# Performance work log

Measured on AMD Instinct MI355X. Metric: run time of the kernel, lower is better.

Reference implementation:

```python
import jax, jax.numpy as jnp
import numpy as np

N_NODES = 100000  # number of bonds (nodes of the bond-graph)
N_EDGES = 500000  # angle edges per head
NUM_ANGLE = 4
BOND_DIM = 128
HIDDEN_DIM = 128  # must equal BOND_DIM (alpha * x_j elementwise)


def setup_inputs() -> dict:
    key = jax.random.key(0)
    k1, k2, k3 = jax.random.split(key, 3)
    bond_feat = jax.random.normal(k1, (N_NODES, BOND_DIM), dtype=jnp.float32)
    edge_index = jax.random.randint(k2, (NUM_ANGLE, 2, N_EDGES), 0, N_NODES, dtype=jnp.int64)
    # attn_fc weight per angle head: Linear(2*bond_dim -> hidden_dim); stored as [in, out]
    W = jax.random.normal(k3, (NUM_ANGLE, 2 * BOND_DIM, HIDDEN_DIM), dtype=jnp.float32) * (1.0 / np.sqrt(2 * BOND_DIM))
    b = jnp.zeros((NUM_ANGLE, HIDDEN_DIM), dtype=jnp.float32)
    return {"bond_feat": bond_feat, "edge_index": edge_index, "W": W, "b": b}


def reference(bond_feat, edge_index, W, b):
    n_nodes = bond_feat.shape[0]

    def one_angle(ei, Wk, bk):
        src, dst = ei[0], ei[1]            # PyG: edge_index[0]=j (source), [1]=i (target)
        x_j = bond_feat[src]               # [E, D]
        x_i = bond_feat[dst]               # [E, D]
        alpha = jnp.tanh(jnp.concatenate([x_i, x_j], axis=-1) @ Wk + bk)  # [E, H]
        msg = alpha * x_j                  # requires H == D
        return jax.ops.segment_sum(msg, dst, num_segments=n_nodes)        # [N, H]

    h = jax.vmap(one_angle)(edge_index, W, b)          # [A, N, H]
    # merge == 'cat': concat heads along feature dim -> [N, A*H]
    feat_h = jnp.transpose(h, (1, 0, 2)).reshape(n_nodes, -1)
    return feat_h
```

## Files before the change

kernel.cpp:

```cpp
#include <hip/hip_runtime.h>
#include <hip/hip_bf16.h>
#include <stdint.h>

#define NN 100000
#define NE 500000
#define NA 4
#define DIM 128
#define LDA 136

#define NBINS (NA * NN)
#define SCAN_CHUNK 1024
#define NBLK ((NBINS + SCAN_CHUNK - 1) / SCAN_CHUNK)

typedef __attribute__((ext_vector_type(8))) short bf16x8;
typedef __attribute__((ext_vector_type(4))) float f32x4;
typedef unsigned short u16;
typedef unsigned int u32;
typedef unsigned long long u64;

__device__ __forceinline__ u16 f2bf(float x) {
    u32 u = __float_as_uint(x);
    u32 r = (u + 0x7fffu + ((u >> 16) & 1u)) >> 16;
    return (u16)r;
}
__device__ __forceinline__ float bf2f(u16 h) {
    return __uint_as_float(((u32)h) << 16);
}
__device__ __forceinline__ float fast_tanh(float x) {
    float t = __expf(2.0f * x);
    return 1.0f - __fdividef(2.0f, t + 1.0f);
}

__global__ __launch_bounds__(256) void cast_bond(const float* __restrict__ x,
                                                 u16* __restrict__ y) {
    int i = blockIdx.x * 256 + threadIdx.x;
    if (i >= NN * DIM / 8) return;
    const float4* xv = (const float4*)x;
    float4 a = xv[2 * i], b = xv[2 * i + 1];
    uint4 o;
    o.x = (u32)f2bf(a.x) | ((u32)f2bf(a.y) << 16);
    o.y = (u32)f2bf(a.z) | ((u32)f2bf(a.w) << 16);
    o.z = (u32)f2bf(b.x) | ((u32)f2bf(b.y) << 16);
    o.w = (u32)f2bf(b.z) | ((u32)f2bf(b.w) << 16);
    ((uint4*)y)[i] = o;
}

__global__ __launch_bounds__(256) void pack_w(const float* __restrict__ W,
                                              u16* __restrict__ WbT) {
    int i = blockIdx.x * 256 + threadIdx.x;
    int d = i & 127;
    int o = (i >> 7) & 127;
    int st = i >> 14;
    WbT[i] = f2bf(W[(size_t)(st * 128 + d) * 128 + o]);
}

__global__ __launch_bounds__(256) void gemm_y(const u16* __restrict__ bondB,
                                              const u16* __restrict__ WbT,
                                              const float* __restrict__ bias,
                                              u16* __restrict__ Y) {
    __shared__ __align__(16) u16 As[64 * LDA];
    __shared__ __align__(16) u16 Bs[128 * LDA];
    const int node0 = blockIdx.x * 64;
    const int tid = threadIdx.x;

#pragma unroll
    for (int it = 0; it < 4; ++it) {
        int idx = it * 256 + tid;
        int row = idx >> 4, ch = idx & 15;
        int gr = node0 + row;
        if (gr >= NN) gr = NN - 1;
        *(uint4*)&As[row * LDA + ch * 8] = *(const uint4*)&bondB[(size_t)gr * DIM + ch * 8];
    }

    const int wave = tid >> 6, lane = tid & 63;
    const int m0 = wave * 16;
    const int lrow = lane & 15;
    const int lk8 = (lane >> 4) * 8;
    const int rbase = (lane >> 4) * 4;

    for (int slab = 0; slab < 8; ++slab) {
        __syncthreads();
        const u16* Wslab = WbT + (size_t)slab * DIM * DIM;
#pragma unroll
        for (int it = 0; it < 8; ++it) {
            int idx = it * 256 + tid;
            *(uint4*)&Bs[(idx >> 4) * LDA + (idx & 15) * 8] = *(const uint4*)&Wslab[idx * 8];
        }
        __syncthreads();

        f32x4 acc[8] = {};
#pragma unroll
        for (int kk = 0; kk < 4; ++kk) {
            int ko = kk * 32 + lk8;
            bf16x8 a = *(const bf16x8*)&As[(m0 + lrow) * LDA + ko];
#pragma unroll
            for (int nb = 0; nb < 8; ++nb) {
                bf16x8 b = *(const bf16x8*)&Bs[(nb * 16 + lrow) * LDA + ko];
                acc[nb] = __builtin_amdgcn_mfma_f32_16x16x32_bf16(a, b, acc[nb], 0, 0, 0);
            }
        }

        const int k = slab >> 1, t = slab & 1;
#pragma unroll
        for (int nb = 0; nb < 8; ++nb) {
            int o = nb * 16 + lrow;
            float bv = (t == 0) ? bias[k * DIM + o] : 0.0f;
#pragma unroll
            for (int r = 0; r < 4; ++r) {
                int node = node0 + m0 + rbase + r;
                if (node < NN)
                    Y[(size_t)slab * NN * DIM + (size_t)node * DIM + o] = f2bf(acc[nb][r] + bv);
            }
        }
    }
}


__global__ __launch_bounds__(256) void hist_kernel(const int* __restrict__ ei,
                                                   int* __restrict__ counts) {
    int k = blockIdx.y;
    int e = blockIdx.x * 256 + threadIdx.x;
    if (e >= NE) return;
    int dst = ei[(size_t)(k * 2 + 1) * NE + e];
    atomicAdd(&counts[k * NN + dst], 1);
}

__global__ __launch_bounds__(256) void scan_reduce(const int* __restrict__ counts,
                                                   int* __restrict__ blockSums) {
    int b = blockIdx.x, t = threadIdx.x;
    int base = b * SCAN_CHUNK + t * 4;
    int s = 0;
#pragma unroll
    for (int u = 0; u < 4; ++u) {
        int i = base + u;
        if (i < NBINS) s += counts[i];
    }
    __shared__ int red[256];
    red[t] = s;
    __syncthreads();
    for (int off = 128; off > 0; off >>= 1) {
        if (t < off) red[t] += red[t + off];
        __syncthreads();
    }
    if (t == 0) blockSums[b] = red[0];
}

__global__ void scan_bases(int* __restrict__ blockSums, int* __restrict__ offsets) {
    __shared__ int lds[512];
    int t = threadIdx.x;
    lds[t] = (t < NBLK) ? blockSums[t] : 0;
    __syncthreads();
    if (t == 0) {
        int run = 0;
        for (int i = 0; i < NBLK; ++i) {
            int v = lds[i];
            lds[i] = run;
            run += v;
        }
        offsets[NBINS] = run;
    }
    __syncthreads();
    if (t < NBLK) blockSums[t] = lds[t];
}

__global__ __launch_bounds__(256) void scan_write(const int* __restrict__ counts,
                                                  const int* __restrict__ blockBases,
                                                  int* __restrict__ offsets,
                                                  int* __restrict__ woff) {
    int b = blockIdx.x, t = threadIdx.x;
    int base = b * SCAN_CHUNK + t * 4;
    int v[4];
    int s = 0;
#pragma unroll
    for (int u = 0; u < 4; ++u) {
        int i = base + u;
        v[u] = (i < NBINS) ? counts[i] : 0;
        s += v[u];
    }
    __shared__ int lds[256];
    lds[t] = s;
    __syncthreads();
    for (int off = 1; off < 256; off <<= 1) {
        int add = (t >= off) ? lds[t - off] : 0;
        __syncthreads();
        lds[t] += add;
        __syncthreads();
    }
    int run = blockBases[b] + lds[t] - s;
#pragma unroll
    for (int u = 0; u < 4; ++u) {
        int i = base + u;
        if (i < NBINS) {
            offsets[i] = run;
            woff[i] = run;
            run += v[u];
        }
    }
}

__global__ __launch_bounds__(256) void scatter_kernel(const int* __restrict__ ei,
                                                      int* __restrict__ woff,
                                                      int* __restrict__ sorted_src) {
    int k = blockIdx.y;
    int e = blockIdx.x * 256 + threadIdx.x;
    if (e >= NE) return;
    int src = ei[(size_t)(k * 2 + 0) * NE + e];
    int dst = ei[(size_t)(k * 2 + 1) * NE + e];
    int pos = atomicAdd(&woff[k * NN + dst], 1);
    sorted_src[pos] = src;
}

__global__ __launch_bounds__(256) void gather_kernel(const int* __restrict__ offsets,
                                                     const int* __restrict__ sorted_src,
                                                     const u16* __restrict__ Y,
                                                     const u16* __restrict__ bondB,
                                                     float* __restrict__ out) {
    const int k = blockIdx.y;
    const int node = blockIdx.x * 4 + (threadIdx.x >> 6);
    const int lane = threadIdx.x & 63;
    const int f = lane * 2;
    const int bin = k * NN + node;

    int base = __builtin_amdgcn_readfirstlane(offsets[bin]);
    int cnt = __builtin_amdgcn_readfirstlane(offsets[bin + 1]) - base;

    const u16* __restrict__ Y1p = Y + (size_t)(2 * k) * NN * DIM;
    const u16* __restrict__ Y2p = Y + (size_t)(2 * k + 1) * NN * DIM;

    const u32 y1 = *(const u32*)&Y1p[(u32)node * DIM + f];
    const float y1a = __uint_as_float(y1 << 16);
    const float y1b = __uint_as_float(y1 & 0xffff0000u);
    float acc0 = 0.0f, acc1 = 0.0f;

#define EDGE(w, x)                                                      \
    {                                                                   \
        float p0 = y1a + __uint_as_float((w) << 16);                    \
        float p1 = y1b + __uint_as_float((w) & 0xffff0000u);            \
        float e0 = __expf(2.0f * p0);                                   \
        float e1 = __expf(2.0f * p1);                                   \
        float d0 = e0 + 1.0f;                                           \
        float d1 = e1 + 1.0f;                                           \
        float r = __fdividef(1.0f, d0 * d1);                            \
        float th0 = fmaf(-2.0f * d1, r, 1.0f);                          \
        float th1 = fmaf(-2.0f * d0, r, 1.0f);                          \
        acc0 = fmaf(th0, __uint_as_float((x) << 16), acc0);             \
        acc1 = fmaf(th1, __uint_as_float((x) & 0xffff0000u), acc1);     \
    }

    while (cnt > 0) {
        const int take = (cnt < 64) ? cnt : 64;
        const int srcl = sorted_src[base + ((lane < take) ? lane : (take - 1))];
        int e = 0;
        for (; e + 4 <= take; e += 4) {
            const int s0 = __builtin_amdgcn_readlane(srcl, e);
            const int s1 = __builtin_amdgcn_readlane(srcl, e + 1);
            const int s2 = __builtin_amdgcn_readlane(srcl, e + 2);
            const int s3 = __builtin_amdgcn_readlane(srcl, e + 3);
            const u32 w0 = *(const u32*)&Y2p[(u32)s0 * DIM + f];
            const u32 x0 = *(const u32*)&bondB[(u32)s0 * DIM + f];
            const u32 w1 = *(const u32*)&Y2p[(u32)s1 * DIM + f];
            const u32 x1 = *(const u32*)&bondB[(u32)s1 * DIM + f];
            const u32 w2 = *(const u32*)&Y2p[(u32)s2 * DIM + f];
            const u32 x2 = *(const u32*)&bondB[(u32)s2 * DIM + f];
            const u32 w3 = *(const u32*)&Y2p[(u32)s3 * DIM + f];
            const u32 x3 = *(const u32*)&bondB[(u32)s3 * DIM + f];
            EDGE(w0, x0);
            EDGE(w1, x1);
            EDGE(w2, x2);
            EDGE(w3, x3);
        }
        for (; e < take; ++e) {
            const int s = __builtin_amdgcn_readlane(srcl, e);
            const u32 w = *(const u32*)&Y2p[(u32)s * DIM + f];
            const u32 x = *(const u32*)&bondB[(u32)s * DIM + f];
            EDGE(w, x);
        }
        base += take;
        cnt -= take;
    }
#undef EDGE

    u64 uv = ((u64)__float_as_uint(acc1) << 32) | (u64)__float_as_uint(acc0);
    __builtin_nontemporal_store(uv, (u64*)(out + (size_t)node * (NA * DIM) + k * DIM + f));
}

__global__ __launch_bounds__(256) void edge_kernel(const int* __restrict__ ei,
                                                   const u16* __restrict__ Y,
                                                   const float* __restrict__ bond,
                                                   float* __restrict__ out) {
    const int k = blockIdx.y;
    const int e = blockIdx.x * 4 + (threadIdx.x >> 6);
    const int lane = threadIdx.x & 63;
    const int src = ei[(size_t)(k * 2 + 0) * NE + e];
    const int dst = ei[(size_t)(k * 2 + 1) * NE + e];
    const int f = lane * 2;
    const u32 y1p = *(const u32*)&Y[((size_t)(k * 2 + 0) * NN + dst) * DIM + f];
    const u32 y2p = *(const u32*)&Y[((size_t)(k * 2 + 1) * NN + src) * DIM + f];
    const float2 xj = *(const float2*)&bond[(size_t)src * DIM + f];
    float p0 = bf2f((u16)(y1p & 0xffffu)) + bf2f((u16)(y2p & 0xffffu));
    float p1 = bf2f((u16)(y1p >> 16)) + bf2f((u16)(y2p >> 16));
    float a0 = fast_tanh(p0);
    float a1 = fast_tanh(p1);
    float* op = out + (size_t)dst * (NA * DIM) + k * DIM + f;
    atomicAdd(op, a0 * xj.x);
    atomicAdd(op + 1, a1 * xj.y);
}

__global__ __launch_bounds__(128) void fallback_edge(const float* __restrict__ bond,
                                                     const int* __restrict__ ei,
                                                     const float* __restrict__ W,
                                                     const float* __restrict__ bias,
                                                     float* __restrict__ out) {
    __shared__ float xi[DIM], xj[DIM];
    const int k = blockIdx.y;
    const int e = blockIdx.x;
    const int o = threadIdx.x;
    const int src = ei[(size_t)(k * 2 + 0) * NE + e];
    const int dst = ei[(size_t)(k * 2 + 1) * NE + e];
    xi[o] = bond[(size_t)dst * DIM + o];
    xj[o] = bond[(size_t)src * DIM + o];
    __syncthreads();
    const float* Wk = W + (size_t)k * 2 * DIM * DIM;
    float acc = bias[k * DIM + o];
    for (int din = 0; din < DIM; ++din) {
        acc += xi[din] * Wk[din * DIM + o];
        acc += xj[din] * Wk[(DIM + din) * DIM + o];
    }
    float alpha = fast_tanh(acc);
    atomicAdd(&out[(size_t)dst * (NA * DIM) + k * DIM + o], alpha * xj[o]);
}

static inline size_t align256(size_t x) { return (x + 255) & ~(size_t)255; }

extern "C" void kernel_launch(void* const* d_in, const int* in_sizes, int n_in,
                              void* d_out, int out_size, void* d_ws, size_t ws_size,
                              hipStream_t stream) {
    const float* bond = (const float*)d_in[0];
    const int* ei = (const int*)d_in[1];
    const float* W = (const float*)d_in[2];
    const float* bias = (const float*)d_in[3];
    float* out = (float*)d_out;

    const size_t wbt_bytes = align256((size_t)NA * 2 * DIM * DIM * 2);
    const size_t bondb_bytes = align256((size_t)NN * DIM * 2);
    const size_t y_bytes = align256((size_t)NA * 2 * NN * DIM * 2);
    const size_t counts_bytes = align256((size_t)NBINS * 4);
    const size_t offsets_bytes = align256(((size_t)NBINS + 1) * 4);
    const size_t woff_bytes = align256((size_t)NBINS * 4);
    const size_t bsum_bytes = align256((size_t)512 * 4);
    const size_t ssrc_bytes = align256((size_t)NA * NE * 4);

    const size_t base_bytes = wbt_bytes + bondb_bytes + y_bytes;
    const size_t full_bytes = base_bytes + counts_bytes + offsets_bytes +
                              woff_bytes + bsum_bytes + ssrc_bytes;

    if (ws_size >= full_bytes) {
        char* p = (char*)d_ws;
        u16* WbT = (u16*)p;                 p += wbt_bytes;
        u16* bondB = (u16*)p;               p += bondb_bytes;
        u16* Y = (u16*)p;                   p += y_bytes;
        int* counts = (int*)p;              p += counts_bytes;
        int* offsets = (int*)p;             p += offsets_bytes;
        int* woff = (int*)p;                p += woff_bytes;
        int* bsum = (int*)p;                p += bsum_bytes;
        int* ssrc = (int*)p;

        pack_w<<<dim3(131072 / 256), 256, 0, stream>>>(W, WbT);
        cast_bond<<<dim3((NN * DIM / 8 + 255) / 256), 256, 0, stream>>>(bond, bondB);
        gemm_y<<<dim3((NN + 63) / 64), 256, 0, stream>>>(bondB, WbT, bias, Y);

        hipMemsetAsync(counts, 0, (size_t)NBINS * 4, stream);
        hist_kernel<<<dim3((NE + 255) / 256, NA), 256, 0, stream>>>(ei, counts);
        scan_reduce<<<dim3(NBLK), 256, 0, stream>>>(counts, bsum);
        scan_bases<<<dim3(1), 512, 0, stream>>>(bsum, offsets);
        scan_write<<<dim3(NBLK), 256, 0, stream>>>(counts, bsum, offsets, woff);
        scatter_kernel<<<dim3((NE + 255) / 256, NA), 256, 0, stream>>>(ei, woff, ssrc);

        gather_kernel<<<dim3(NN / 4, NA), 256, 0, stream>>>(offsets, ssrc, Y, bondB, out);
    } else if (ws_size >= base_bytes) {
        u16* WbT = (u16*)d_ws;
        u16* bondB = (u16*)((char*)d_ws + wbt_bytes);
        u16* Y = (u16*)((char*)d_ws + wbt_bytes + bondb_bytes);
        hipMemsetAsync(d_out, 0, (size_t)out_size * sizeof(float), stream);
        pack_w<<<dim3(131072 / 256), 256, 0, stream>>>(W, WbT);
        cast_bond<<<dim3((NN * DIM / 8 + 255) / 256), 256, 0, stream>>>(bond, bondB);
        gemm_y<<<dim3((NN + 63) / 64), 256, 0, stream>>>(bondB, WbT, bias, Y);
        edge_kernel<<<dim3(NE / 4, NA), 256, 0, stream>>>(ei, Y, bond, out);
    } else {
        hipMemsetAsync(d_out, 0, (size_t)out_size * sizeof(float), stream);
        fallback_edge<<<dim3(NE, NA), 128, 0, stream>>>(bond, ei, W, bias, out);
    }
}
```

Measured before the change: 763.5 us.

## Fuse cast/pack kernels, parallelize block scan, gather four nodes per wavefront

Merges the bf16 cast of bond features and the weight packing into one launch to save a kernel launch. Replaces the serial single-thread scan over block sums with a parallel Hillis-Steele scan in shared memory. The gather kernel now processes four consecutive destination nodes per wavefront, loading their offsets with one vector read and sharing 64-entry chunks of sorted source indices across node boundaries. This cuts per-node index loads and launches fewer blocks, at the cost of more serial work per wave and padded workspace buffers.

```diff
diff --git a/kernel.cpp b/kernel.cpp
--- a/kernel.cpp
+++ b/kernel.cpp
@@ -11,6 +11,7 @@
 #define NBINS (NA * NN)
 #define SCAN_CHUNK 1024
 #define NBLK ((NBINS + SCAN_CHUNK - 1) / SCAN_CHUNK)
+#define NEDGE_TOT (NA * NE)
 
 typedef __attribute__((ext_vector_type(8))) short bf16x8;
 typedef __attribute__((ext_vector_type(4))) float f32x4;
@@ -31,27 +32,29 @@
     return 1.0f - __fdividef(2.0f, t + 1.0f);
 }
 
-__global__ __launch_bounds__(256) void cast_bond(const float* __restrict__ x,
-                                                 u16* __restrict__ y) {
-    int i = blockIdx.x * 256 + threadIdx.x;
-    if (i >= NN * DIM / 8) return;
-    const float4* xv = (const float4*)x;
-    float4 a = xv[2 * i], b = xv[2 * i + 1];
-    uint4 o;
-    o.x = (u32)f2bf(a.x) | ((u32)f2bf(a.y) << 16);
-    o.y = (u32)f2bf(a.z) | ((u32)f2bf(a.w) << 16);
-    o.z = (u32)f2bf(b.x) | ((u32)f2bf(b.y) << 16);
-    o.w = (u32)f2bf(b.z) | ((u32)f2bf(b.w) << 16);
-    ((uint4*)y)[i] = o;
-}
-
-__global__ __launch_bounds__(256) void pack_w(const float* __restrict__ W,
-                                              u16* __restrict__ WbT) {
-    int i = blockIdx.x * 256 + threadIdx.x;
-    int d = i & 127;
-    int o = (i >> 7) & 127;
-    int st = i >> 14;
-    WbT[i] = f2bf(W[(size_t)(st * 128 + d) * 128 + o]);
+#define CAST_BLKS 6250
+#define PACK_BLKS 512
+__global__ __launch_bounds__(256) void cast_pack(const float* __restrict__ x,
+                                                 u16* __restrict__ y,
+                                                 const float* __restrict__ W,
+                                                 u16* __restrict__ WbT) {
+    if (blockIdx.x < CAST_BLKS) {
+        int i = blockIdx.x * 256 + threadIdx.x;
+        const float4* xv = (const float4*)x;
+        float4 a = xv[2 * i], b = xv[2 * i + 1];
+        uint4 o;
+        o.x = (u32)f2bf(a.x) | ((u32)f2bf(a.y) << 16);
+        o.y = (u32)f2bf(a.z) | ((u32)f2bf(a.w) << 16);
+        o.z = (u32)f2bf(b.x) | ((u32)f2bf(b.y) << 16);
+        o.w = (u32)f2bf(b.z) | ((u32)f2bf(b.w) << 16);
+        ((uint4*)y)[i] = o;
+    } else {
+        int i = (blockIdx.x - CAST_BLKS) * 256 + threadIdx.x;
+        int d = i & 127;
+        int o = (i >> 7) & 127;
+        int st = i >> 14;
+        WbT[i] = f2bf(W[(size_t)(st * 128 + d) * 128 + o]);
+    }
 }
 
 __global__ __launch_bounds__(256) void gemm_y(const u16* __restrict__ bondB,
@@ -150,17 +153,14 @@
     int t = threadIdx.x;
     lds[t] = (t < NBLK) ? blockSums[t] : 0;
     __syncthreads();
-    if (t == 0) {
-        int run = 0;
-        for (int i = 0; i < NBLK; ++i) {
-            int v = lds[i];
-            lds[i] = run;
-            run += v;
-        }
-        offsets[NBINS] = run;
-    }
-    __syncthreads();
-    if (t < NBLK) blockSums[t] = lds[t];
+    for (int off = 1; off < 512; off <<= 1) {
+        int v = (t >= off) ? lds[t - off] : 0;
+        __syncthreads();
+        lds[t] += v;
+        __syncthreads();
+    }
+    if (t < NBLK) blockSums[t] = (t == 0) ? 0 : lds[t - 1];
+    if (t == 0) offsets[NBINS] = lds[NBLK - 1];
 }
 
 __global__ __launch_bounds__(256) void scan_write(const int* __restrict__ counts,
@@ -216,21 +216,35 @@
                                                      const u16* __restrict__ bondB,
                                                      float* __restrict__ out) {
     const int k = blockIdx.y;
-    const int node = blockIdx.x * 4 + (threadIdx.x >> 6);
+    const int wid = threadIdx.x >> 6;
+    const int node0 = blockIdx.x * 16 + wid * 4;
     const int lane = threadIdx.x & 63;
     const int f = lane * 2;
-    const int bin = k * NN + node;
-
-    int base = __builtin_amdgcn_readfirstlane(offsets[bin]);
-    int cnt = __builtin_amdgcn_readfirstlane(offsets[bin + 1]) - base;
+    const int bin0 = k * NN + node0;
+
+    const int4 ob = *(const int4*)&offsets[bin0];
+    const int o0 = __builtin_amdgcn_readfirstlane(ob.x);
+    const int o1 = __builtin_amdgcn_readfirstlane(ob.y);
+    const int o2 = __builtin_amdgcn_readfirstlane(ob.z);
+    const int o3 = __builtin_amdgcn_readfirstlane(ob.w);
+    const int o4 = __builtin_amdgcn_readfirstlane(offsets[bin0 + 4]);
 
     const u16* __restrict__ Y1p = Y + (size_t)(2 * k) * NN * DIM;
     const u16* __restrict__ Y2p = Y + (size_t)(2 * k + 1) * NN * DIM;
 
-    const u32 y1 = *(const u32*)&Y1p[(u32)node * DIM + f];
-    const float y1a = __uint_as_float(y1 << 16);
-    const float y1b = __uint_as_float(y1 & 0xffff0000u);
-    float acc0 = 0.0f, acc1 = 0.0f;
+    u32 y1v[4];
+#pragma unroll
+    for (int b = 0; b < 4; ++b)
+        y1v[b] = *(const u32*)&Y1p[(u32)(node0 + b) * DIM + f];
+
+    int chunkBase = o0;
+    int chunkEnd = o0 + 64;
+    int g0 = chunkBase + lane;
+    g0 = (g0 < NEDGE_TOT) ? g0 : (NEDGE_TOT - 1);
+    int srcl = sorted_src[g0];
+
+    const int ends[4] = {o1, o2, o3, o4};
+    int m = o0;
 
 #define EDGE(w, x)                                                      \
     {                                                                   \
@@ -247,41 +261,54 @@
         acc1 = fmaf(th1, __uint_as_float((x) & 0xffff0000u), acc1);     \
     }
 
-    while (cnt > 0) {
-        const int take = (cnt < 64) ? cnt : 64;
-        const int srcl = sorted_src[base + ((lane < take) ? lane : (take - 1))];
-        int e = 0;
-        for (; e + 4 <= take; e += 4) {
-            const int s0 = __builtin_amdgcn_readlane(srcl, e);
-            const int s1 = __builtin_amdgcn_readlane(srcl, e + 1);
-            const int s2 = __builtin_amdgcn_readlane(srcl, e + 2);
-            const int s3 = __builtin_amdgcn_readlane(srcl, e + 3);
-            const u32 w0 = *(const u32*)&Y2p[(u32)s0 * DIM + f];
-            const u32 x0 = *(const u32*)&bondB[(u32)s0 * DIM + f];
-            const u32 w1 = *(const u32*)&Y2p[(u32)s1 * DIM + f];
-            const u32 x1 = *(const u32*)&bondB[(u32)s1 * DIM + f];
-            const u32 w2 = *(const u32*)&Y2p[(u32)s2 * DIM + f];
-            const u32 x2 = *(const u32*)&bondB[(u32)s2 * DIM + f];
-            const u32 w3 = *(const u32*)&Y2p[(u32)s3 * DIM + f];
-            const u32 x3 = *(const u32*)&bondB[(u32)s3 * DIM + f];
-            EDGE(w0, x0);
-            EDGE(w1, x1);
-            EDGE(w2, x2);
-            EDGE(w3, x3);
+#pragma unroll
+    for (int b = 0; b < 4; ++b) {
+        const float y1a = __uint_as_float(y1v[b] << 16);
+        const float y1b = __uint_as_float(y1v[b] & 0xffff0000u);
+        const int e_end = ends[b];
+        float acc0 = 0.0f, acc1 = 0.0f;
+
+        while (m < e_end) {
+            if (m >= chunkEnd) {
+                chunkBase = m;
+                chunkEnd = m + 64;
+                int g = chunkBase + lane;
+                g = (g < NEDGE_TOT) ? g : (NEDGE_TOT - 1);
+                srcl = sorted_src[g];
+            }
+            const int lim = (e_end < chunkEnd) ? e_end : chunkEnd;
+            for (; m + 4 <= lim; m += 4) {
+                const int idx = m - chunkBase;
+                const int s0 = __builtin_amdgcn_readlane(srcl, idx);
+                const int s1 = __builtin_amdgcn_readlane(srcl, idx + 1);
+                const int s2 = __builtin_amdgcn_readlane(srcl, idx + 2);
+                const int s3 = __builtin_amdgcn_readlane(srcl, idx + 3);
+                const u32 w0 = *(const u32*)&Y2p[(u32)s0 * DIM + f];
+                const u32 x0 = *(const u32*)&bondB[(u32)s0 * DIM + f];
+                const u32 w1 = *(const u32*)&Y2p[(u32)s1 * DIM + f];
+                const u32 x1 = *(const u32*)&bondB[(u32)s1 * DIM + f];
+                const u32 w2 = *(const u32*)&Y2p[(u32)s2 * DIM + f];
+                const u32 x2 = *(const u32*)&bondB[(u32)s2 * DIM + f];
+                const u32 w3 = *(const u32*)&Y2p[(u32)s3 * DIM + f];
+                const u32 x3 = *(const u32*)&bondB[(u32)s3 * DIM + f];
+                EDGE(w0, x0);
+                EDGE(w1, x1);
+                EDGE(w2, x2);
+                EDGE(w3, x3);
+            }
+            for (; m < lim; ++m) {
+                const int s = __builtin_amdgcn_readlane(srcl, m - chunkBase);
+                const u32 w = *(const u32*)&Y2p[(u32)s * DIM + f];
+                const u32 x = *(const u32*)&bondB[(u32)s * DIM + f];
+                EDGE(w, x);
+            }
         }
-        for (; e < take; ++e) {
-            const int s = __builtin_amdgcn_readlane(srcl, e);
-            const u32 w = *(const u32*)&Y2p[(u32)s * DIM + f];
-            const u32 x = *(const u32*)&bondB[(u32)s * DIM + f];
-            EDGE(w, x);
-        }
-        base += take;
-        cnt -= take;
+
+        u64 uv = ((u64)__float_as_uint(acc1) << 32) | (u64)__float_as_uint(acc0);
+        __builtin_nontemporal_store(
+            uv, (u64*)(out + (size_t)(node0 + b) * (NA * DIM) + k * DIM + f));
     }
 #undef EDGE
-
-    u64 uv = ((u64)__float_as_uint(acc1) << 32) | (u64)__float_as_uint(acc0);
-    __builtin_nontemporal_store(uv, (u64*)(out + (size_t)node * (NA * DIM) + k * DIM + f));
 }
 
 __global__ __launch_bounds__(256) void edge_kernel(const int* __restrict__ ei,
@@ -345,10 +372,10 @@
     const size_t bondb_bytes = align256((size_t)NN * DIM * 2);
     const size_t y_bytes = align256((size_t)NA * 2 * NN * DIM * 2);
     const size_t counts_bytes = align256((size_t)NBINS * 4);
-    const size_t offsets_bytes = align256(((size_t)NBINS + 1) * 4);
+    const size_t offsets_bytes = align256(((size_t)NBINS + 8) * 4);
     const size_t woff_bytes = align256((size_t)NBINS * 4);
     const size_t bsum_bytes = align256((size_t)512 * 4);
-    const size_t ssrc_bytes = align256((size_t)NA * NE * 4);
+    const size_t ssrc_bytes = align256((size_t)NA * NE * 4 + 256);
 
     const size_t base_bytes = wbt_bytes + bondb_bytes + y_bytes;
     const size_t full_bytes = base_bytes + counts_bytes + offsets_bytes +
@@ -365,8 +392,7 @@
         int* bsum = (int*)p;                p += bsum_bytes;
         int* ssrc = (int*)p;
 
-        pack_w<<<dim3(131072 / 256), 256, 0, stream>>>(W, WbT);
-        cast_bond<<<dim3((NN * DIM / 8 + 255) / 256), 256, 0, stream>>>(bond, bondB);
+        cast_pack<<<dim3(CAST_BLKS + PACK_BLKS), 256, 0, stream>>>(bond, bondB, W, WbT);
         gemm_y<<<dim3((NN + 63) / 64), 256, 0, stream>>>(bondB, WbT, bias, Y);
 
         hipMemsetAsync(counts, 0, (size_t)NBINS * 4, stream);
@@ -376,14 +402,13 @@
         scan_write<<<dim3(NBLK), 256, 0, stream>>>(counts, bsum, offsets, woff);
         scatter_kernel<<<dim3((NE + 255) / 256, NA), 256, 0, stream>>>(ei, woff, ssrc);
 
-        gather_kernel<<<dim3(NN / 4, NA), 256, 0, stream>>>(offsets, ssrc, Y, bondB, out);
+        gather_kernel<<<dim3(NN / 16, NA), 256, 0, stream>>>(offsets, ssrc, Y, bondB, out);
     } else if (ws_size >= base_bytes) {
         u16* WbT = (u16*)d_ws;
         u16* bondB = (u16*)((char*)d_ws + wbt_bytes);
         u16* Y = (u16*)((char*)d_ws + wbt_bytes + bondb_bytes);
         hipMemsetAsync(d_out, 0, (size_t)out_size * sizeof(float), stream);
-        pack_w<<<dim3(131072 / 256), 256, 0, stream>>>(W, WbT);
-        cast_bond<<<dim3((NN * DIM / 8 + 255) / 256), 256, 0, stream>>>(bond, bondB);
+        cast_pack<<<dim3(CAST_BLKS + PACK_BLKS), 256, 0, stream>>>(bond, bondB, W, WbT);
         gemm_y<<<dim3((NN + 63) / 64), 256, 0, stream>>>(bondB, WbT, bias, Y);
         edge_kernel<<<dim3(NE / 4, NA), 256, 0, stream>>>(ei, Y, bond, out);
     } else {
```

After: 748.4 us. 2.0% less time.
